# Kernel tuning notes

Measured on AMD Instinct MI355X. Metric: run time of the kernel, lower is better.

Reference implementation:

```python
import jax, jax.numpy as jnp
import numpy as np

TEMPERATURE = 0.1
NEG_INF = -1e9  # finite large-negative so logsumexp/grads stay NaN-free
EPS = 1e-12


def setup_inputs() -> dict:
    key = jax.random.key(0)
    k1, k2, k3, k4 = jax.random.split(key, 4)
    N, D = 8192, 256
    return {
        "embeddings": jax.random.normal(k1, (N, D), dtype=jnp.float32),
        "labels": jax.random.randint(k2, (N,), 0, 2048, dtype=jnp.int32),
        "graph_ids": jax.random.randint(k3, (N,), 0, 16, dtype=jnp.int32),
        "categories": jax.random.randint(k4, (N,), 0, 6, dtype=jnp.int32),
    }


def reference(embeddings, labels, graph_ids, categories):
    N = embeddings.shape[0]
    # L2-normalize rows (torch F.normalize with eps clamp)
    norms = jnp.linalg.norm(embeddings, axis=1, keepdims=True)
    E = embeddings / jnp.maximum(norms, EPS)
    # Full cosine-similarity matrix [N, N] (module materializes N^2 anyway)
    S = E @ E.T

    same_label = labels[:, None] == labels[None, :]
    same_graph = graph_ids[:, None] == graph_ids[None, :]
    cons = categories < 3
    cons_ij = cons[:, None] & cons[None, :]

    # ---- positive-pair (1 - cos_sim) term: i<j, same label, diff graph, both conserved
    pos_full = same_label & (~same_graph) & cons_ij
    upper = jnp.triu(jnp.ones((N, N), dtype=bool), k=1)
    pair_mask = pos_full & upper
    n_pairs = pair_mask.sum()
    pos_loss = jnp.where(
        n_pairs > 0,
        jnp.sum(jnp.where(pair_mask, 1.0 - S, 0.0)) / jnp.maximum(n_pairs, 1).astype(S.dtype),
        0.0,
    )

    # ---- supervised InfoNCE (max_negatives=0 => subset = participating nodes)
    participating = pos_full.any(axis=0) | pos_full.any(axis=1)
    part_ij = participating[:, None] & participating[None, :]
    neg_mask = (~same_graph) & (~same_label)
    diag = jnp.eye(N, dtype=bool)
    valid = (pos_full | neg_mask) & part_ij & (~diag)

    logits = jnp.where(valid, S / TEMPERATURE, NEG_INF)
    lse = jax.nn.logsumexp(logits, axis=1)  # [N]; rows w/o valid entries never hit pos_full
    n_pos = pos_full.sum()
    nce_loss = jnp.where(
        n_pos > 0,
        jnp.sum(jnp.where(pos_full, lse[:, None] - logits, 0.0)) / jnp.maximum(n_pos, 1).astype(S.dtype),
        0.0,
    )
    return pos_loss + nce_loss
```

## Files before the change

### kernel.cpp

```cpp
#include <hip/hip_runtime.h>
#include <hip/hip_bf16.h>

#define N_NODES 8192
#define DIM 256
#define NLAB 2048
#define NGRAPH 16
#define NSLICE 16
#define INV_T 10.0f

typedef __attribute__((ext_vector_type(8))) short short8;
typedef __attribute__((ext_vector_type(4))) float f32x4;

__device__ __forceinline__ ushort f2bf(float f) {
    uint u = __float_as_uint(f);
    return (ushort)((u + 0x7FFFu + ((u >> 16) & 1u)) >> 16);
}

__global__ void k_counts(const int* __restrict__ labels, const int* __restrict__ graphs,
                         const int* __restrict__ cats, int* __restrict__ cnt, int* __restrict__ tot) {
    int i = blockIdx.x * 256 + threadIdx.x;
    if (i >= N_NODES) return;
    if (cats[i] < 3) {
        atomicAdd(&cnt[labels[i] * NGRAPH + graphs[i]], 1);
        atomicAdd(&tot[labels[i]], 1);
    }
}

__global__ void k_compact(const int* __restrict__ labels, const int* __restrict__ graphs,
                          const int* __restrict__ cats, const int* __restrict__ cnt,
                          const int* __restrict__ tot, int* P_count, int* n_pos,
                          int* __restrict__ idx_c, int* __restrict__ meta,
                          int* __restrict__ rc_c) {
    int i = blockIdx.x * 256 + threadIdx.x;
    if (i >= N_NODES) return;
    if (cats[i] < 3) {
        int l = labels[i], g = graphs[i];
        int rc = tot[l] - cnt[l * NGRAPH + g];
        if (rc > 0) {
            int p = atomicAdd(P_count, 1);
            idx_c[p] = i;
            meta[p] = (l << 4) | g;
            rc_c[p] = rc;
            atomicAdd(n_pos, rc);
        }
    }
}

__global__ __launch_bounds__(256) void k_gather(const float* __restrict__ emb,
                                                const int* __restrict__ P_count,
                                                const int* __restrict__ idx_c,
                                                ushort* __restrict__ Epb) {
    int w = threadIdx.x >> 6, lane = threadIdx.x & 63;
    int p = blockIdx.x * 4 + w;
    int P = *P_count;
    ushort4 o = make_ushort4(0, 0, 0, 0);
    if (p < P) {
        int row = idx_c[p];
        float4 v = *(const float4*)&emb[(size_t)row * DIM + lane * 4];
        float ss = v.x * v.x + v.y * v.y + v.z * v.z + v.w * v.w;
        #pragma unroll
        for (int off = 32; off; off >>= 1) ss += __shfl_xor(ss, off, 64);
        float inv = 1.0f / fmaxf(sqrtf(ss), 1e-12f);
        o.x = f2bf(v.x * inv); o.y = f2bf(v.y * inv);
        o.z = f2bf(v.z * inv); o.w = f2bf(v.w * inv);
    }
    *(ushort4*)&Epb[(size_t)p * DIM + lane * 4] = o;
}

__global__ __launch_bounds__(256) void k_main(
    const ushort* __restrict__ Epb, const int* __restrict__ P_count,
    const int* __restrict__ meta, float* __restrict__ s_glob, float* __restrict__ pos_glob) {
    __shared__ ushort sm[64 * 256];
    int P = *P_count;
    int rt = blockIdx.x;
    int ntiles = (P + 63) >> 6;
    if (rt >= ntiles) return;
    int slice = blockIdx.y;
    int t = threadIdx.x;
    int w = t >> 6, l = t & 63;
    int rowbase = rt * 64;

    #pragma unroll
    for (int it = 0; it < 8; ++it) {
        int u = it * 256 + t;
        int G = u >> 6, l6 = u & 63;
        int rl = l6 & 15, sub = l6 >> 4;
        int r = rowbase + (G >> 3) * 16 + rl;
        int k0 = (G & 7) * 32 + sub * 8;
        uint4 v = *(const uint4*)&Epb[(size_t)r * DIM + k0];
        *(uint4*)&sm[u * 8] = v;
    }
    __syncthreads();
    short8 af[2][8];
    #pragma unroll
    for (int rg = 0; rg < 2; ++rg) {
        int rgi = (w & 1) * 2 + rg;
        #pragma unroll
        for (int ks = 0; ks < 8; ++ks)
            af[rg][ks] = *(const short8*)&sm[((rgi * 8 + ks) * 64 + l) * 8];
    }
    int mp[8];
    #pragma unroll
    for (int rg = 0; rg < 2; ++rg)
        #pragma unroll
        for (int j = 0; j < 4; ++j)
            mp[rg * 4 + j] = meta[rowbase + (w & 1) * 32 + rg * 16 + (l >> 4) * 4 + j];

    float s_acc[8] = {0.f, 0.f, 0.f, 0.f, 0.f, 0.f, 0.f, 0.f};
    float p_acc[8] = {0.f, 0.f, 0.f, 0.f, 0.f, 0.f, 0.f, 0.f};
    int cgi0 = (w >> 1) * 2, cgi1 = cgi0 + 1;
    __syncthreads();

    for (int ct = slice; ct < ntiles; ct += NSLICE) {
        int colbase = ct * 64;
        #pragma unroll
        for (int it = 0; it < 8; ++it) {
            int u = it * 256 + t;
            int G = u >> 6, l6 = u & 63;
            int rl = l6 & 15, sub = l6 >> 4;
            int r = colbase + (G >> 3) * 16 + rl;
            int k0 = (G & 7) * 32 + sub * 8;
            uint4 v = *(const uint4*)&Epb[(size_t)r * DIM + k0];
            *(uint4*)&sm[u * 8] = v;
        }
        __syncthreads();
        f32x4 acc00 = {0.f, 0.f, 0.f, 0.f}, acc01 = {0.f, 0.f, 0.f, 0.f};
        f32x4 acc10 = {0.f, 0.f, 0.f, 0.f}, acc11 = {0.f, 0.f, 0.f, 0.f};
        #pragma unroll
        for (int ks = 0; ks < 8; ++ks) {
            short8 b0 = *(const short8*)&sm[((cgi0 * 8 + ks) * 64 + l) * 8];
            short8 b1 = *(const short8*)&sm[((cgi1 * 8 + ks) * 64 + l) * 8];
            acc00 = __builtin_amdgcn_mfma_f32_16x16x32_bf16(af[0][ks], b0, acc00, 0, 0, 0);
            acc01 = __builtin_amdgcn_mfma_f32_16x16x32_bf16(af[0][ks], b1, acc01, 0, 0, 0);
            acc10 = __builtin_amdgcn_mfma_f32_16x16x32_bf16(af[1][ks], b0, acc10, 0, 0, 0);
            acc11 = __builtin_amdgcn_mfma_f32_16x16x32_bf16(af[1][ks], b1, acc11, 0, 0, 0);
        }
        #pragma unroll
        for (int cg = 0; cg < 2; ++cg) {
            int q = colbase + (cgi0 + cg) * 16 + (l & 15);
            bool vq = q < P;
            int mq = meta[q];
            #pragma unroll
            for (int rg = 0; rg < 2; ++rg) {
                f32x4 a = (rg == 0) ? (cg == 0 ? acc00 : acc01)
                                    : (cg == 0 ? acc10 : acc11);
                #pragma unroll
                for (int j = 0; j < 4; ++j) {
                    float sv = a[j];
                    int mpv = mp[rg * 4 + j];
                    bool val = vq && (((mq ^ mpv) & 15) != 0);
                    float e = __expf(sv * INV_T);
                    s_acc[rg * 4 + j] += val ? e : 0.f;
                    p_acc[rg * 4 + j] += (val && ((mq >> 4) == (mpv >> 4))) ? sv : 0.f;
                }
            }
        }
        __syncthreads();
    }

    #pragma unroll
    for (int off = 1; off < 16; off <<= 1)
        #pragma unroll
        for (int i = 0; i < 8; ++i) {
            s_acc[i] += __shfl_xor(s_acc[i], off, 64);
            p_acc[i] += __shfl_xor(p_acc[i], off, 64);
        }
    if ((l & 15) == 0) {
        #pragma unroll
        for (int rg = 0; rg < 2; ++rg)
            #pragma unroll
            for (int j = 0; j < 4; ++j) {
                int p = rowbase + (w & 1) * 32 + rg * 16 + (l >> 4) * 4 + j;
                if (p < P) {
                    atomicAdd(&s_glob[p], s_acc[rg * 4 + j]);
                    atomicAdd(&pos_glob[p], p_acc[rg * 4 + j]);
                }
            }
    }
}

__global__ __launch_bounds__(256) void k_reduce(
    const int* __restrict__ P_count, const int* __restrict__ n_pos_p,
    const int* __restrict__ rc_c, const float* __restrict__ s_glob,
    const float* __restrict__ pos_glob, float* __restrict__ out) {
    __shared__ float red[256];
    __shared__ float red2[256];
    int P = *P_count;
    float nce_local = 0.f, pos_local = 0.f;
    for (int p = threadIdx.x; p < P; p += 256) {
        float lse = logf(s_glob[p]);
        nce_local += (float)rc_c[p] * lse;
        pos_local += pos_glob[p];
    }
    red[threadIdx.x] = nce_local;
    red2[threadIdx.x] = pos_local;
    __syncthreads();
    for (int wd = 128; wd; wd >>= 1) {
        if (threadIdx.x < (unsigned)wd) {
            red[threadIdx.x] += red[threadIdx.x + wd];
            red2[threadIdx.x] += red2[threadIdx.x + wd];
        }
        __syncthreads();
    }
    if (threadIdx.x == 0) {
        int npos = *n_pos_p;
        float result = 0.f;
        if (npos > 0) {
            float possum = red2[0];
            float n_pairs = (float)(npos / 2);
            float pos_loss = (n_pairs - 0.5f * possum) / n_pairs;
            float nce = (red[0] - possum * INV_T) / (float)npos;
            result = pos_loss + nce;
        }
        out[0] = result;
    }
}

extern "C" void kernel_launch(void* const* d_in, const int* in_sizes, int n_in,
                              void* d_out, int out_size, void* d_ws, size_t ws_size,
                              hipStream_t stream) {
    const float* emb  = (const float*)d_in[0];
    const int* labels = (const int*)d_in[1];
    const int* graphs = (const int*)d_in[2];
    const int* cats   = (const int*)d_in[3];

    char* ws = (char*)d_ws;
    size_t off = 0;
    ushort* Epb = (ushort*)(ws + off); off += (size_t)N_NODES * DIM * 2;
    int* cnt     = (int*)(ws + off); off += NLAB * NGRAPH * 4;
    int* tot     = (int*)(ws + off); off += NLAB * 4;
    int* P_count = (int*)(ws + off); off += 4;
    int* n_pos   = (int*)(ws + off); off += 4;
    size_t zero1 = (size_t)NLAB * NGRAPH * 4 + NLAB * 4 + 8;
    off = (off + 255) & ~(size_t)255;
    int* idx_c = (int*)(ws + off); off += N_NODES * 4;
    int* rc_c  = (int*)(ws + off); off += N_NODES * 4;
    int* meta  = (int*)(ws + off); off += N_NODES * 4;
    float* s_glob   = (float*)(ws + off); off += N_NODES * 4;
    float* pos_glob = (float*)(ws + off); off += N_NODES * 4;

    hipMemsetAsync(cnt, 0, zero1, stream);
    hipMemsetAsync(s_glob, 0, (size_t)N_NODES * 8, stream);
    k_counts<<<N_NODES / 256, 256, 0, stream>>>(labels, graphs, cats, cnt, tot);
    k_compact<<<N_NODES / 256, 256, 0, stream>>>(labels, graphs, cats, cnt, tot,
                                                 P_count, n_pos, idx_c, meta, rc_c);
    k_gather<<<N_NODES / 4, 256, 0, stream>>>(emb, P_count, idx_c, Epb);
    dim3 grid(N_NODES / 64, NSLICE);
    k_main<<<grid, 256, 0, stream>>>(Epb, P_count, meta, s_glob, pos_glob);
    k_reduce<<<1, 256, 0, stream>>>(P_count, n_pos, rc_c, s_glob, pos_glob, (float*)d_out);
}
```

Baseline: 114.1 us.

## Fuse all pipeline stages into one cooperative persistent kernel with grid syncs

Replaces the two memsets and five kernel launches with a single cooperative kernel that zeroes the workspace, counts, compacts, normalizes and gathers, runs the MFMA similarity pass over persistent blocks, and reduces to the scalar output, with grid.sync between stages. The goal is to remove per-launch overhead and inter-kernel gaps. The cost is that the main pass now runs on a limited number of resident blocks (at most 512), which loop over tile items instead of a full grid, and each grid.sync adds latency. The original multi-kernel path is kept as a fallback if the cooperative launch fails.

```diff
diff --git a/kernel.cpp b/kernel.cpp
--- a/kernel.cpp
+++ b/kernel.cpp
@@ -1,12 +1,18 @@
 #include <hip/hip_runtime.h>
 #include <hip/hip_bf16.h>
+#include <hip/hip_cooperative_groups.h>
+
+namespace cg = cooperative_groups;
 
 #define N_NODES 8192
 #define DIM 256
 #define NLAB 2048
 #define NGRAPH 16
 #define NSLICE 16
+#define NT 256
+#define NB_MAX 512
 #define INV_T 10.0f
+#define ZN_INTS (NLAB * NGRAPH + NLAB + 4 + 2 * N_NODES)
 
 typedef __attribute__((ext_vector_type(8))) short short8;
 typedef __attribute__((ext_vector_type(4))) float f32x4;
@@ -14,6 +20,232 @@
 __device__ __forceinline__ ushort f2bf(float f) {
     uint u = __float_as_uint(f);
     return (ushort)((u + 0x7FFFu + ((u >> 16) & 1u)) >> 16);
+}
+
+
+__global__ __launch_bounds__(NT, 2) void k_fused(
+    const float* __restrict__ emb, const int* __restrict__ labels,
+    const int* __restrict__ graphs, const int* __restrict__ cats,
+    char* __restrict__ ws, float* __restrict__ out) {
+    __shared__ ushort sm[64 * 256];
+    cg::grid_group grid = cg::this_grid();
+
+    ushort* Epb    = (ushort*)ws;
+    int* zbase     = (int*)(ws + (size_t)N_NODES * DIM * 2);
+    int* cnt       = zbase;
+    int* tot       = cnt + NLAB * NGRAPH;
+    int* P_count   = tot + NLAB;
+    int* n_pos     = P_count + 1;
+    float* acc_nce = (float*)(n_pos + 1);
+    float* acc_pos = acc_nce + 1;
+    float* s_glob  = acc_pos + 1;
+    float* pos_glob= s_glob + N_NODES;
+    int* idx_c     = (int*)(pos_glob + N_NODES);
+    int* rc_c      = idx_c + N_NODES;
+    int* meta      = rc_c + N_NODES;
+
+    const int bid = blockIdx.x, tid = threadIdx.x;
+    const int gtid = bid * NT + tid;
+    const int nthreads = gridDim.x * NT;
+
+    for (int i = gtid; i < ZN_INTS; i += nthreads) zbase[i] = 0;
+    grid.sync();
+
+    for (int i = gtid; i < N_NODES; i += nthreads) {
+        if (cats[i] < 3) {
+            atomicAdd(&cnt[labels[i] * NGRAPH + graphs[i]], 1);
+            atomicAdd(&tot[labels[i]], 1);
+        }
+    }
+    grid.sync();
+
+    for (int i = gtid; i < N_NODES; i += nthreads) {
+        if (cats[i] < 3) {
+            int lb = labels[i], g = graphs[i];
+            int rc = tot[lb] - cnt[lb * NGRAPH + g];
+            if (rc > 0) {
+                int p = atomicAdd(P_count, 1);
+                idx_c[p] = i;
+                meta[p] = (lb << 4) | g;
+                rc_c[p] = rc;
+                atomicAdd(n_pos, rc);
+            }
+        }
+    }
+    __threadfence();
+    grid.sync();
+
+    const int P = *P_count;
+    const int ntiles = (P + 63) >> 6;
+
+    {
+        int nwaves = nthreads >> 6;
+        int wv = gtid >> 6, lane = gtid & 63;
+        int prows = ntiles * 64;
+        for (int p = wv; p < prows; p += nwaves) {
+            ushort4 o = make_ushort4(0, 0, 0, 0);
+            if (p < P) {
+                int row = idx_c[p];
+                float4 v = *(const float4*)&emb[(size_t)row * DIM + lane * 4];
+                float ss = v.x * v.x + v.y * v.y + v.z * v.z + v.w * v.w;
+                #pragma unroll
+                for (int off = 32; off; off >>= 1) ss += __shfl_xor(ss, off, 64);
+                float inv = 1.0f / fmaxf(sqrtf(ss), 1e-12f);
+                o.x = f2bf(v.x * inv); o.y = f2bf(v.y * inv);
+                o.z = f2bf(v.z * inv); o.w = f2bf(v.w * inv);
+            }
+            *(ushort4*)&Epb[(size_t)p * DIM + lane * 4] = o;
+        }
+    }
+    __threadfence();
+    grid.sync();
+
+    {
+        const int w = tid >> 6, l = tid & 63;
+        const int nitems = ntiles * NSLICE;
+        for (int item = bid; item < nitems; item += gridDim.x) {
+            int rt = item >> 4;
+            int slice = item & (NSLICE - 1);
+            int rowbase = rt * 64;
+
+            #pragma unroll
+            for (int it = 0; it < 8; ++it) {
+                int u = it * 256 + tid;
+                int G = u >> 6, l6 = u & 63;
+                int rl = l6 & 15, sub = l6 >> 4;
+                int r = rowbase + (G >> 3) * 16 + rl;
+                int k0 = (G & 7) * 32 + sub * 8;
+                uint4 v = *(const uint4*)&Epb[(size_t)r * DIM + k0];
+                *(uint4*)&sm[u * 8] = v;
+            }
+            __syncthreads();
+            short8 af[2][8];
+            #pragma unroll
+            for (int rg = 0; rg < 2; ++rg) {
+                int rgi = (w & 1) * 2 + rg;
+                #pragma unroll
+                for (int ks = 0; ks < 8; ++ks)
+                    af[rg][ks] = *(const short8*)&sm[((rgi * 8 + ks) * 64 + l) * 8];
+            }
+            int mp[8];
+            #pragma unroll
+            for (int rg = 0; rg < 2; ++rg)
+                #pragma unroll
+                for (int j = 0; j < 4; ++j)
+                    mp[rg * 4 + j] = meta[rowbase + (w & 1) * 32 + rg * 16 + (l >> 4) * 4 + j];
+
+            float s_acc[8] = {0.f, 0.f, 0.f, 0.f, 0.f, 0.f, 0.f, 0.f};
+            float p_acc[8] = {0.f, 0.f, 0.f, 0.f, 0.f, 0.f, 0.f, 0.f};
+            int cgi0 = (w >> 1) * 2, cgi1 = cgi0 + 1;
+            __syncthreads();
+
+            for (int ct = slice; ct < ntiles; ct += NSLICE) {
+                int colbase = ct * 64;
+                #pragma unroll
+                for (int it = 0; it < 8; ++it) {
+                    int u = it * 256 + tid;
+                    int G = u >> 6, l6 = u & 63;
+                    int rl = l6 & 15, sub = l6 >> 4;
+                    int r = colbase + (G >> 3) * 16 + rl;
+                    int k0 = (G & 7) * 32 + sub * 8;
+                    uint4 v = *(const uint4*)&Epb[(size_t)r * DIM + k0];
+                    *(uint4*)&sm[u * 8] = v;
+                }
+                __syncthreads();
+                f32x4 acc00 = {0.f, 0.f, 0.f, 0.f}, acc01 = {0.f, 0.f, 0.f, 0.f};
+                f32x4 acc10 = {0.f, 0.f, 0.f, 0.f}, acc11 = {0.f, 0.f, 0.f, 0.f};
+                #pragma unroll
+                for (int ks = 0; ks < 8; ++ks) {
+                    short8 b0 = *(const short8*)&sm[((cgi0 * 8 + ks) * 64 + l) * 8];
+                    short8 b1 = *(const short8*)&sm[((cgi1 * 8 + ks) * 64 + l) * 8];
+                    acc00 = __builtin_amdgcn_mfma_f32_16x16x32_bf16(af[0][ks], b0, acc00, 0, 0, 0);
+                    acc01 = __builtin_amdgcn_mfma_f32_16x16x32_bf16(af[0][ks], b1, acc01, 0, 0, 0);
+                    acc10 = __builtin_amdgcn_mfma_f32_16x16x32_bf16(af[1][ks], b0, acc10, 0, 0, 0);
+                    acc11 = __builtin_amdgcn_mfma_f32_16x16x32_bf16(af[1][ks], b1, acc11, 0, 0, 0);
+                }
+                #pragma unroll
+                for (int cg2 = 0; cg2 < 2; ++cg2) {
+                    int q = colbase + (cgi0 + cg2) * 16 + (l & 15);
+                    bool vq = q < P;
+                    int mq = meta[q];
+                    #pragma unroll
+                    for (int rg = 0; rg < 2; ++rg) {
+                        f32x4 a = (rg == 0) ? (cg2 == 0 ? acc00 : acc01)
+                                            : (cg2 == 0 ? acc10 : acc11);
+                        #pragma unroll
+                        for (int j = 0; j < 4; ++j) {
+                            float sv = a[j];
+                            int mpv = mp[rg * 4 + j];
+                            bool val = vq && (((mq ^ mpv) & 15) != 0);
+                            float e = __expf(sv * INV_T);
+                            s_acc[rg * 4 + j] += val ? e : 0.f;
+                            p_acc[rg * 4 + j] += (val && ((mq >> 4) == (mpv >> 4))) ? sv : 0.f;
+                        }
+                    }
+                }
+                __syncthreads();
+            }
+            #pragma unroll
+            for (int off = 1; off < 16; off <<= 1)
+                #pragma unroll
+                for (int i = 0; i < 8; ++i) {
+                    s_acc[i] += __shfl_xor(s_acc[i], off, 64);
+                    p_acc[i] += __shfl_xor(p_acc[i], off, 64);
+                }
+            if ((l & 15) == 0) {
+                #pragma unroll
+                for (int rg = 0; rg < 2; ++rg)
+                    #pragma unroll
+                    for (int j = 0; j < 4; ++j) {
+                        int p = rowbase + (w & 1) * 32 + rg * 16 + (l >> 4) * 4 + j;
+                        if (p < P) {
+                            atomicAdd(&s_glob[p], s_acc[rg * 4 + j]);
+                            atomicAdd(&pos_glob[p], p_acc[rg * 4 + j]);
+                        }
+                    }
+            }
+        }
+    }
+    __threadfence();
+    grid.sync();
+
+    {
+        float nce_l = 0.f, pos_l = 0.f;
+        for (int p = gtid; p < P; p += nthreads) {
+            nce_l += (float)rc_c[p] * logf(s_glob[p]);
+            pos_l += pos_glob[p];
+        }
+        float* red = (float*)sm;
+        red[tid] = nce_l;
+        red[NT + tid] = pos_l;
+        __syncthreads();
+        for (int wd = 128; wd; wd >>= 1) {
+            if (tid < wd) {
+                red[tid] += red[tid + wd];
+                red[NT + tid] += red[NT + tid + wd];
+            }
+            __syncthreads();
+        }
+        if (tid == 0) {
+            atomicAdd(acc_nce, red[0]);
+            atomicAdd(acc_pos, red[NT]);
+        }
+    }
+    __threadfence();
+    grid.sync();
+
+    if (gtid == 0) {
+        int npos = *n_pos;
+        float result = 0.f;
+        if (npos > 0) {
+            float possum = *acc_pos;
+            float n_pairs = (float)(npos / 2);
+            float pos_loss = (n_pairs - 0.5f * possum) / n_pairs;
+            float nce = (*acc_nce - possum * INV_T) / (float)npos;
+            result = pos_loss + nce;
+        }
+        out[0] = result;
+    }
 }
 
 __global__ void k_counts(const int* __restrict__ labels, const int* __restrict__ graphs,
@@ -136,14 +368,14 @@
             acc11 = __builtin_amdgcn_mfma_f32_16x16x32_bf16(af[1][ks], b1, acc11, 0, 0, 0);
         }
         #pragma unroll
-        for (int cg = 0; cg < 2; ++cg) {
-            int q = colbase + (cgi0 + cg) * 16 + (l & 15);
+        for (int cg2 = 0; cg2 < 2; ++cg2) {
+            int q = colbase + (cgi0 + cg2) * 16 + (l & 15);
             bool vq = q < P;
             int mq = meta[q];
             #pragma unroll
             for (int rg = 0; rg < 2; ++rg) {
-                f32x4 a = (rg == 0) ? (cg == 0 ? acc00 : acc01)
-                                    : (cg == 0 ? acc10 : acc11);
+                f32x4 a = (rg == 0) ? (cg2 == 0 ? acc00 : acc01)
+                                    : (cg2 == 0 ? acc10 : acc11);
                 #pragma unroll
                 for (int j = 0; j < 4; ++j) {
                     float sv = a[j];
@@ -157,7 +389,6 @@
         }
         __syncthreads();
     }
-
     #pragma unroll
     for (int off = 1; off < 16; off <<= 1)
         #pragma unroll
@@ -183,22 +414,20 @@
     const int* __restrict__ P_count, const int* __restrict__ n_pos_p,
     const int* __restrict__ rc_c, const float* __restrict__ s_glob,
     const float* __restrict__ pos_glob, float* __restrict__ out) {
-    __shared__ float red[256];
-    __shared__ float red2[256];
+    __shared__ float red[512];
     int P = *P_count;
     float nce_local = 0.f, pos_local = 0.f;
     for (int p = threadIdx.x; p < P; p += 256) {
-        float lse = logf(s_glob[p]);
-        nce_local += (float)rc_c[p] * lse;
+        nce_local += (float)rc_c[p] * logf(s_glob[p]);
         pos_local += pos_glob[p];
     }
     red[threadIdx.x] = nce_local;
-    red2[threadIdx.x] = pos_local;
+    red[256 + threadIdx.x] = pos_local;
     __syncthreads();
     for (int wd = 128; wd; wd >>= 1) {
         if (threadIdx.x < (unsigned)wd) {
             red[threadIdx.x] += red[threadIdx.x + wd];
-            red2[threadIdx.x] += red2[threadIdx.x + wd];
+            red[256 + threadIdx.x] += red[256 + threadIdx.x + wd];
         }
         __syncthreads();
     }
@@ -206,7 +435,7 @@
         int npos = *n_pos_p;
         float result = 0.f;
         if (npos > 0) {
-            float possum = red2[0];
+            float possum = red[256];
             float n_pairs = (float)(npos / 2);
             float pos_loss = (n_pairs - 0.5f * possum) / n_pairs;
             float nce = (red[0] - possum * INV_T) / (float)npos;
@@ -223,29 +452,53 @@
     const int* labels = (const int*)d_in[1];
     const int* graphs = (const int*)d_in[2];
     const int* cats   = (const int*)d_in[3];
-
-    char* ws = (char*)d_ws;
-    size_t off = 0;
-    ushort* Epb = (ushort*)(ws + off); off += (size_t)N_NODES * DIM * 2;
-    int* cnt     = (int*)(ws + off); off += NLAB * NGRAPH * 4;
-    int* tot     = (int*)(ws + off); off += NLAB * 4;
-    int* P_count = (int*)(ws + off); off += 4;
-    int* n_pos   = (int*)(ws + off); off += 4;
-    size_t zero1 = (size_t)NLAB * NGRAPH * 4 + NLAB * 4 + 8;
-    off = (off + 255) & ~(size_t)255;
-    int* idx_c = (int*)(ws + off); off += N_NODES * 4;
-    int* rc_c  = (int*)(ws + off); off += N_NODES * 4;
-    int* meta  = (int*)(ws + off); off += N_NODES * 4;
-    float* s_glob   = (float*)(ws + off); off += N_NODES * 4;
-    float* pos_glob = (float*)(ws + off); off += N_NODES * 4;
-
-    hipMemsetAsync(cnt, 0, zero1, stream);
-    hipMemsetAsync(s_glob, 0, (size_t)N_NODES * 8, stream);
-    k_counts<<<N_NODES / 256, 256, 0, stream>>>(labels, graphs, cats, cnt, tot);
-    k_compact<<<N_NODES / 256, 256, 0, stream>>>(labels, graphs, cats, cnt, tot,
-                                                 P_count, n_pos, idx_c, meta, rc_c);
-    k_gather<<<N_NODES / 4, 256, 0, stream>>>(emb, P_count, idx_c, Epb);
-    dim3 grid(N_NODES / 64, NSLICE);
-    k_main<<<grid, 256, 0, stream>>>(Epb, P_count, meta, s_glob, pos_glob);
-    k_reduce<<<1, 256, 0, stream>>>(P_count, n_pos, rc_c, s_glob, pos_glob, (float*)d_out);
-}
+    char* ws   = (char*)d_ws;
+    float* outp = (float*)d_out;
+
+    ushort* Epb    = (ushort*)ws;
+    int* zbase     = (int*)(ws + (size_t)N_NODES * DIM * 2);
+    int* cnt       = zbase;
+    int* tot       = cnt + NLAB * NGRAPH;
+    int* P_count   = tot + NLAB;
+    int* n_pos     = P_count + 1;
+    float* acc_nce = (float*)(n_pos + 1);
+    float* acc_pos = acc_nce + 1;
+    float* s_glob  = acc_pos + 1;
+    float* pos_glob= s_glob + N_NODES;
+    int* idx_c     = (int*)(pos_glob + N_NODES);
+    int* rc_c      = idx_c + N_NODES;
+    int* meta      = rc_c + N_NODES;
+    (void)acc_nce; (void)acc_pos;
+
+    int devId = 0;
+    (void)hipGetDevice(&devId);
+    int blocksPerCU = 0, numCU = 0;
+    hipError_t occErr = hipOccupancyMaxActiveBlocksPerMultiprocessor(
+        &blocksPerCU, (const void*)k_fused, NT, 0);
+    hipError_t attrErr = hipDeviceGetAttribute(
+        &numCU, hipDeviceAttributeMultiprocessorCount, devId);
+
+    int nb = 0;
+    if (occErr == hipSuccess && attrErr == hipSuccess && blocksPerCU > 0 && numCU > 0) {
+        nb = blocksPerCU * numCU;
+        if (nb > NB_MAX) nb = NB_MAX;
+    }
+
+    hipError_t launchErr = hipErrorUnknown;
+    if (nb > 0) {
+        void* args[6] = {(void*)&emb, (void*)&labels, (void*)&graphs,
+                         (void*)&cats, (void*)&ws, (void*)&outp};
+        launchErr = hipLaunchCooperativeKernel((const void*)k_fused, dim3(nb), dim3(NT),
+                                               args, 0, stream);
+    }
+    if (launchErr != hipSuccess) {
+        hipMemsetAsync(zbase, 0, (size_t)ZN_INTS * 4, stream);
+        k_counts<<<N_NODES / 256, 256, 0, stream>>>(labels, graphs, cats, cnt, tot);
+        k_compact<<<N_NODES / 256, 256, 0, stream>>>(labels, graphs, cats, cnt, tot,
+                                                     P_count, n_pos, idx_c, meta, rc_c);
+        k_gather<<<N_NODES / 4, 256, 0, stream>>>(emb, P_count, idx_c, Epb);
+        dim3 grid(N_NODES / 64, NSLICE);
+        k_main<<<grid, 256, 0, stream>>>(Epb, P_count, meta, s_glob, pos_glob);
+        k_reduce<<<1, 256, 0, stream>>>(P_count, n_pos, rc_c, s_glob, pos_glob, outp);
+    }
+}
```

Measured after the change: 393.6 us. 245% more time.

## Fuse prep kernels and memsets, fold final reduction into main kernel

Applied to the files above, without the earlier changes.

Replaces the two memsets plus the counts and compact kernels with one single-block kernel that zeroes the workspace and does both passes behind block barriers. The separate reduce kernel is folded into the main kernel with a last-block-done atomic counter. Together these cut the number of launches from seven to three. The cost is that the prep work now runs on a single 1024-thread block, and the main kernel adds a threadfence and an atomic counter per block.

```diff
diff --git a/kernel.cpp b/kernel.cpp
--- a/kernel.cpp
+++ b/kernel.cpp
@@ -7,6 +7,7 @@
 #define NGRAPH 16
 #define NSLICE 16
 #define INV_T 10.0f
+#define ZN_INTS (NLAB * NGRAPH + NLAB + 3 + 2 * N_NODES)
 
 typedef __attribute__((ext_vector_type(8))) short short8;
 typedef __attribute__((ext_vector_type(4))) float f32x4;
@@ -16,40 +17,55 @@
     return (ushort)((u + 0x7FFFu + ((u >> 16) & 1u)) >> 16);
 }
 
-__global__ void k_counts(const int* __restrict__ labels, const int* __restrict__ graphs,
-                         const int* __restrict__ cats, int* __restrict__ cnt, int* __restrict__ tot) {
-    int i = blockIdx.x * 256 + threadIdx.x;
-    if (i >= N_NODES) return;
-    if (cats[i] < 3) {
-        atomicAdd(&cnt[labels[i] * NGRAPH + graphs[i]], 1);
-        atomicAdd(&tot[labels[i]], 1);
-    }
-}
-
-__global__ void k_compact(const int* __restrict__ labels, const int* __restrict__ graphs,
-                          const int* __restrict__ cats, const int* __restrict__ cnt,
-                          const int* __restrict__ tot, int* P_count, int* n_pos,
-                          int* __restrict__ idx_c, int* __restrict__ meta,
-                          int* __restrict__ rc_c) {
-    int i = blockIdx.x * 256 + threadIdx.x;
-    if (i >= N_NODES) return;
-    if (cats[i] < 3) {
-        int l = labels[i], g = graphs[i];
-        int rc = tot[l] - cnt[l * NGRAPH + g];
-        if (rc > 0) {
-            int p = atomicAdd(P_count, 1);
-            idx_c[p] = i;
-            meta[p] = (l << 4) | g;
-            rc_c[p] = rc;
-            atomicAdd(n_pos, rc);
+__global__ __launch_bounds__(1024) void k_prep(
+    const int* __restrict__ labels, const int* __restrict__ graphs,
+    const int* __restrict__ cats, char* __restrict__ ws) {
+    int* zbase   = (int*)(ws + (size_t)N_NODES * DIM * 2);
+    int* cnt     = zbase;
+    int* tot     = cnt + NLAB * NGRAPH;
+    int* P_count = tot + NLAB;
+    int* n_pos   = P_count + 1;
+    int* idx_c   = zbase + ZN_INTS;
+    int* rc_c    = idx_c + N_NODES;
+    int* meta    = rc_c + N_NODES;
+
+    const int tid = threadIdx.x;
+
+    for (int i = tid; i < ZN_INTS; i += 1024) zbase[i] = 0;
+    __syncthreads();
+
+    for (int i = tid; i < N_NODES; i += 1024) {
+        if (cats[i] < 3) {
+            atomicAdd(&cnt[labels[i] * NGRAPH + graphs[i]], 1);
+            atomicAdd(&tot[labels[i]], 1);
+        }
+    }
+    __syncthreads();
+
+    for (int i = tid; i < N_NODES; i += 1024) {
+        if (cats[i] < 3) {
+            int lb = labels[i], g = graphs[i];
+            int c  = atomicAdd(&cnt[lb * NGRAPH + g], 0);
+            int tt = atomicAdd(&tot[lb], 0);
+            int rc = tt - c;
+            if (rc > 0) {
+                int p = atomicAdd(P_count, 1);
+                idx_c[p] = i;
+                meta[p] = (lb << 4) | g;
+                rc_c[p] = rc;
+                atomicAdd(n_pos, rc);
+            }
         }
     }
 }
 
 __global__ __launch_bounds__(256) void k_gather(const float* __restrict__ emb,
-                                                const int* __restrict__ P_count,
-                                                const int* __restrict__ idx_c,
-                                                ushort* __restrict__ Epb) {
+                                                char* __restrict__ ws) {
+    ushort* Epb  = (ushort*)ws;
+    int* zbase   = (int*)(ws + (size_t)N_NODES * DIM * 2);
+    int* P_count = zbase + NLAB * NGRAPH + NLAB;
+    int* idx_c   = zbase + ZN_INTS;
+
     int w = threadIdx.x >> 6, lane = threadIdx.x & 63;
     int p = blockIdx.x * 4 + w;
     int P = *P_count;
@@ -67,152 +83,170 @@
     *(ushort4*)&Epb[(size_t)p * DIM + lane * 4] = o;
 }
 
-__global__ __launch_bounds__(256) void k_main(
-    const ushort* __restrict__ Epb, const int* __restrict__ P_count,
-    const int* __restrict__ meta, float* __restrict__ s_glob, float* __restrict__ pos_glob) {
+__global__ __launch_bounds__(256) void k_mainred(char* __restrict__ ws, float* __restrict__ out) {
     __shared__ ushort sm[64 * 256];
-    int P = *P_count;
-    int rt = blockIdx.x;
-    int ntiles = (P + 63) >> 6;
-    if (rt >= ntiles) return;
-    int slice = blockIdx.y;
-    int t = threadIdx.x;
-    int w = t >> 6, l = t & 63;
-    int rowbase = rt * 64;
-
-    #pragma unroll
-    for (int it = 0; it < 8; ++it) {
-        int u = it * 256 + t;
-        int G = u >> 6, l6 = u & 63;
-        int rl = l6 & 15, sub = l6 >> 4;
-        int r = rowbase + (G >> 3) * 16 + rl;
-        int k0 = (G & 7) * 32 + sub * 8;
-        uint4 v = *(const uint4*)&Epb[(size_t)r * DIM + k0];
-        *(uint4*)&sm[u * 8] = v;
-    }
-    __syncthreads();
-    short8 af[2][8];
-    #pragma unroll
-    for (int rg = 0; rg < 2; ++rg) {
-        int rgi = (w & 1) * 2 + rg;
-        #pragma unroll
-        for (int ks = 0; ks < 8; ++ks)
-            af[rg][ks] = *(const short8*)&sm[((rgi * 8 + ks) * 64 + l) * 8];
-    }
-    int mp[8];
-    #pragma unroll
-    for (int rg = 0; rg < 2; ++rg)
-        #pragma unroll
-        for (int j = 0; j < 4; ++j)
-            mp[rg * 4 + j] = meta[rowbase + (w & 1) * 32 + rg * 16 + (l >> 4) * 4 + j];
-
-    float s_acc[8] = {0.f, 0.f, 0.f, 0.f, 0.f, 0.f, 0.f, 0.f};
-    float p_acc[8] = {0.f, 0.f, 0.f, 0.f, 0.f, 0.f, 0.f, 0.f};
-    int cgi0 = (w >> 1) * 2, cgi1 = cgi0 + 1;
-    __syncthreads();
-
-    for (int ct = slice; ct < ntiles; ct += NSLICE) {
-        int colbase = ct * 64;
+    __shared__ int is_last;
+
+    ushort* Epb    = (ushort*)ws;
+    int* zbase     = (int*)(ws + (size_t)N_NODES * DIM * 2);
+    int* cnt       = zbase;
+    int* tot       = cnt + NLAB * NGRAPH;
+    int* P_count   = tot + NLAB;
+    int* n_pos     = P_count + 1;
+    int* done      = n_pos + 1;
+    float* s_glob  = (float*)(done + 1);
+    float* pos_glob= s_glob + N_NODES;
+    int* idx_c     = zbase + ZN_INTS;
+    int* rc_c      = idx_c + N_NODES;
+    int* meta      = rc_c + N_NODES;
+    (void)idx_c;
+
+    const int P = *P_count;
+    const int ntiles = (P + 63) >> 6;
+    const int rt = blockIdx.x;
+    const int slice = blockIdx.y;
+    const int t = threadIdx.x;
+    const int w = t >> 6, l = t & 63;
+
+    if (rt < ntiles) {
+        int rowbase = rt * 64;
         #pragma unroll
         for (int it = 0; it < 8; ++it) {
             int u = it * 256 + t;
             int G = u >> 6, l6 = u & 63;
             int rl = l6 & 15, sub = l6 >> 4;
-            int r = colbase + (G >> 3) * 16 + rl;
+            int r = rowbase + (G >> 3) * 16 + rl;
             int k0 = (G & 7) * 32 + sub * 8;
             uint4 v = *(const uint4*)&Epb[(size_t)r * DIM + k0];
             *(uint4*)&sm[u * 8] = v;
         }
         __syncthreads();
-        f32x4 acc00 = {0.f, 0.f, 0.f, 0.f}, acc01 = {0.f, 0.f, 0.f, 0.f};
-        f32x4 acc10 = {0.f, 0.f, 0.f, 0.f}, acc11 = {0.f, 0.f, 0.f, 0.f};
-        #pragma unroll
-        for (int ks = 0; ks < 8; ++ks) {
-            short8 b0 = *(const short8*)&sm[((cgi0 * 8 + ks) * 64 + l) * 8];
-            short8 b1 = *(const short8*)&sm[((cgi1 * 8 + ks) * 64 + l) * 8];
-            acc00 = __builtin_amdgcn_mfma_f32_16x16x32_bf16(af[0][ks], b0, acc00, 0, 0, 0);
-            acc01 = __builtin_amdgcn_mfma_f32_16x16x32_bf16(af[0][ks], b1, acc01, 0, 0, 0);
-            acc10 = __builtin_amdgcn_mfma_f32_16x16x32_bf16(af[1][ks], b0, acc10, 0, 0, 0);
-            acc11 = __builtin_amdgcn_mfma_f32_16x16x32_bf16(af[1][ks], b1, acc11, 0, 0, 0);
-        }
-        #pragma unroll
-        for (int cg = 0; cg < 2; ++cg) {
-            int q = colbase + (cgi0 + cg) * 16 + (l & 15);
-            bool vq = q < P;
-            int mq = meta[q];
-            #pragma unroll
-            for (int rg = 0; rg < 2; ++rg) {
-                f32x4 a = (rg == 0) ? (cg == 0 ? acc00 : acc01)
-                                    : (cg == 0 ? acc10 : acc11);
+        short8 af[2][8];
+        #pragma unroll
+        for (int rg = 0; rg < 2; ++rg) {
+            int rgi = (w & 1) * 2 + rg;
+            #pragma unroll
+            for (int ks = 0; ks < 8; ++ks)
+                af[rg][ks] = *(const short8*)&sm[((rgi * 8 + ks) * 64 + l) * 8];
+        }
+        int mp[8];
+        #pragma unroll
+        for (int rg = 0; rg < 2; ++rg)
+            #pragma unroll
+            for (int j = 0; j < 4; ++j)
+                mp[rg * 4 + j] = meta[rowbase + (w & 1) * 32 + rg * 16 + (l >> 4) * 4 + j];
+
+        float s_acc[8] = {0.f, 0.f, 0.f, 0.f, 0.f, 0.f, 0.f, 0.f};
+        float p_acc[8] = {0.f, 0.f, 0.f, 0.f, 0.f, 0.f, 0.f, 0.f};
+        int cgi0 = (w >> 1) * 2, cgi1 = cgi0 + 1;
+        __syncthreads();
+
+        for (int ct = slice; ct < ntiles; ct += NSLICE) {
+            int colbase = ct * 64;
+            #pragma unroll
+            for (int it = 0; it < 8; ++it) {
+                int u = it * 256 + t;
+                int G = u >> 6, l6 = u & 63;
+                int rl = l6 & 15, sub = l6 >> 4;
+                int r = colbase + (G >> 3) * 16 + rl;
+                int k0 = (G & 7) * 32 + sub * 8;
+                uint4 v = *(const uint4*)&Epb[(size_t)r * DIM + k0];
+                *(uint4*)&sm[u * 8] = v;
+            }
+            __syncthreads();
+            f32x4 acc00 = {0.f, 0.f, 0.f, 0.f}, acc01 = {0.f, 0.f, 0.f, 0.f};
+            f32x4 acc10 = {0.f, 0.f, 0.f, 0.f}, acc11 = {0.f, 0.f, 0.f, 0.f};
+            #pragma unroll
+            for (int ks = 0; ks < 8; ++ks) {
+                short8 b0 = *(const short8*)&sm[((cgi0 * 8 + ks) * 64 + l) * 8];
+                short8 b1 = *(const short8*)&sm[((cgi1 * 8 + ks) * 64 + l) * 8];
+                acc00 = __builtin_amdgcn_mfma_f32_16x16x32_bf16(af[0][ks], b0, acc00, 0, 0, 0);
+                acc01 = __builtin_amdgcn_mfma_f32_16x16x32_bf16(af[0][ks], b1, acc01, 0, 0, 0);
+                acc10 = __builtin_amdgcn_mfma_f32_16x16x32_bf16(af[1][ks], b0, acc10, 0, 0, 0);
+                acc11 = __builtin_amdgcn_mfma_f32_16x16x32_bf16(af[1][ks], b1, acc11, 0, 0, 0);
+            }
+            #pragma unroll
+            for (int cg2 = 0; cg2 < 2; ++cg2) {
+                int q = colbase + (cgi0 + cg2) * 16 + (l & 15);
+                bool vq = q < P;
+                int mq = meta[q];
+                #pragma unroll
+                for (int rg = 0; rg < 2; ++rg) {
+                    f32x4 a = (rg == 0) ? (cg2 == 0 ? acc00 : acc01)
+                                        : (cg2 == 0 ? acc10 : acc11);
+                    #pragma unroll
+                    for (int j = 0; j < 4; ++j) {
+                        float sv = a[j];
+                        int mpv = mp[rg * 4 + j];
+                        bool val = vq && (((mq ^ mpv) & 15) != 0);
+                        float e = __expf(sv * INV_T);
+                        s_acc[rg * 4 + j] += val ? e : 0.f;
+                        p_acc[rg * 4 + j] += (val && ((mq >> 4) == (mpv >> 4))) ? sv : 0.f;
+                    }
+                }
+            }
+            __syncthreads();
+        }
+        #pragma unroll
+        for (int off = 1; off < 16; off <<= 1)
+            #pragma unroll
+            for (int i = 0; i < 8; ++i) {
+                s_acc[i] += __shfl_xor(s_acc[i], off, 64);
+                p_acc[i] += __shfl_xor(p_acc[i], off, 64);
+            }
+        if ((l & 15) == 0) {
+            #pragma unroll
+            for (int rg = 0; rg < 2; ++rg)
                 #pragma unroll
                 for (int j = 0; j < 4; ++j) {
-                    float sv = a[j];
-                    int mpv = mp[rg * 4 + j];
-                    bool val = vq && (((mq ^ mpv) & 15) != 0);
-                    float e = __expf(sv * INV_T);
-                    s_acc[rg * 4 + j] += val ? e : 0.f;
-                    p_acc[rg * 4 + j] += (val && ((mq >> 4) == (mpv >> 4))) ? sv : 0.f;
+                    int p = rowbase + (w & 1) * 32 + rg * 16 + (l >> 4) * 4 + j;
+                    if (p < P) {
+                        atomicAdd(&s_glob[p], s_acc[rg * 4 + j]);
+                        atomicAdd(&pos_glob[p], p_acc[rg * 4 + j]);
+                    }
                 }
-            }
-        }
+        }
+    }
+
+    __threadfence();
+    __syncthreads();
+    if (t == 0) {
+        int total = gridDim.x * gridDim.y;
+        int old = atomicAdd(done, 1);
+        is_last = (old == total - 1) ? 1 : 0;
+    }
+    __syncthreads();
+    if (is_last) {
+        float nce_l = 0.f, pos_l = 0.f;
+        for (int p = t; p < P; p += 256) {
+            float sv = atomicAdd(&s_glob[p], 0.f);
+            float pv = atomicAdd(&pos_glob[p], 0.f);
+            nce_l += (float)rc_c[p] * logf(sv);
+            pos_l += pv;
+        }
+        float* red = (float*)sm;
+        red[t] = nce_l;
+        red[256 + t] = pos_l;
         __syncthreads();
-    }
-
-    #pragma unroll
-    for (int off = 1; off < 16; off <<= 1)
-        #pragma unroll
-        for (int i = 0; i < 8; ++i) {
-            s_acc[i] += __shfl_xor(s_acc[i], off, 64);
-            p_acc[i] += __shfl_xor(p_acc[i], off, 64);
-        }
-    if ((l & 15) == 0) {
-        #pragma unroll
-        for (int rg = 0; rg < 2; ++rg)
-            #pragma unroll
-            for (int j = 0; j < 4; ++j) {
-                int p = rowbase + (w & 1) * 32 + rg * 16 + (l >> 4) * 4 + j;
-                if (p < P) {
-                    atomicAdd(&s_glob[p], s_acc[rg * 4 + j]);
-                    atomicAdd(&pos_glob[p], p_acc[rg * 4 + j]);
-                }
-            }
-    }
-}
-
-__global__ __launch_bounds__(256) void k_reduce(
-    const int* __restrict__ P_count, const int* __restrict__ n_pos_p,
-    const int* __restrict__ rc_c, const float* __restrict__ s_glob,
-    const float* __restrict__ pos_glob, float* __restrict__ out) {
-    __shared__ float red[256];
-    __shared__ float red2[256];
-    int P = *P_count;
-    float nce_local = 0.f, pos_local = 0.f;
-    for (int p = threadIdx.x; p < P; p += 256) {
-        float lse = logf(s_glob[p]);
-        nce_local += (float)rc_c[p] * lse;
-        pos_local += pos_glob[p];
-    }
-    red[threadIdx.x] = nce_local;
-    red2[threadIdx.x] = pos_local;
-    __syncthreads();
-    for (int wd = 128; wd; wd >>= 1) {
-        if (threadIdx.x < (unsigned)wd) {
-            red[threadIdx.x] += red[threadIdx.x + wd];
-            red2[threadIdx.x] += red2[threadIdx.x + wd];
-        }
-        __syncthreads();
-    }
-    if (threadIdx.x == 0) {
-        int npos = *n_pos_p;
-        float result = 0.f;
-        if (npos > 0) {
-            float possum = red2[0];
-            float n_pairs = (float)(npos / 2);
-            float pos_loss = (n_pairs - 0.5f * possum) / n_pairs;
-            float nce = (red[0] - possum * INV_T) / (float)npos;
-            result = pos_loss + nce;
-        }
-        out[0] = result;
+        for (int wd = 128; wd; wd >>= 1) {
+            if (t < wd) {
+                red[t] += red[t + wd];
+                red[256 + t] += red[256 + t + wd];
+            }
+            __syncthreads();
+        }
+        if (t == 0) {
+            int npos = *n_pos;
+            float result = 0.f;
+            if (npos > 0) {
+                float possum = red[256];
+                float n_pairs = (float)(npos / 2);
+                float pos_loss = (n_pairs - 0.5f * possum) / n_pairs;
+                float nce = (red[0] - possum * INV_T) / (float)npos;
+                result = pos_loss + nce;
+            }
+            out[0] = result;
+        }
     }
 }
 
@@ -223,29 +257,11 @@
     const int* labels = (const int*)d_in[1];
     const int* graphs = (const int*)d_in[2];
     const int* cats   = (const int*)d_in[3];
-
-    char* ws = (char*)d_ws;
-    size_t off = 0;
-    ushort* Epb = (ushort*)(ws + off); off += (size_t)N_NODES * DIM * 2;
-    int* cnt     = (int*)(ws + off); off += NLAB * NGRAPH * 4;
-    int* tot     = (int*)(ws + off); off += NLAB * 4;
-    int* P_count = (int*)(ws + off); off += 4;
-    int* n_pos   = (int*)(ws + off); off += 4;
-    size_t zero1 = (size_t)NLAB * NGRAPH * 4 + NLAB * 4 + 8;
-    off = (off + 255) & ~(size_t)255;
-    int* idx_c = (int*)(ws + off); off += N_NODES * 4;
-    int* rc_c  = (int*)(ws + off); off += N_NODES * 4;
-    int* meta  = (int*)(ws + off); off += N_NODES * 4;
-    float* s_glob   = (float*)(ws + off); off += N_NODES * 4;
-    float* pos_glob = (float*)(ws + off); off += N_NODES * 4;
-
-    hipMemsetAsync(cnt, 0, zero1, stream);
-    hipMemsetAsync(s_glob, 0, (size_t)N_NODES * 8, stream);
-    k_counts<<<N_NODES / 256, 256, 0, stream>>>(labels, graphs, cats, cnt, tot);
-    k_compact<<<N_NODES / 256, 256, 0, stream>>>(labels, graphs, cats, cnt, tot,
-                                                 P_count, n_pos, idx_c, meta, rc_c);
-    k_gather<<<N_NODES / 4, 256, 0, stream>>>(emb, P_count, idx_c, Epb);
+    char* ws    = (char*)d_ws;
+    float* outp = (float*)d_out;
+
+    k_prep<<<1, 1024, 0, stream>>>(labels, graphs, cats, ws);
+    k_gather<<<N_NODES / 4, 256, 0, stream>>>(emb, ws);
     dim3 grid(N_NODES / 64, NSLICE);
-    k_main<<<grid, 256, 0, stream>>>(Epb, P_count, meta, s_glob, pos_glob);
-    k_reduce<<<1, 256, 0, stream>>>(P_count, n_pos, rc_c, s_glob, pos_glob, (float*)d_out);
-}
+    k_mainred<<<grid, 256, 0, stream>>>(ws, outp);
+}
```

Result: slower. 268.1 us (+134.9%).
